# Kernel optimization log

Measured on AMD Instinct MI355X. Metric: run time of the kernel, lower is better.

Reference implementation:

```python
import jax, jax.numpy as jnp
import numpy as np

N, G, L, C = 32768, 128, 256, 128   # nodes, graphs, nodes-per-graph, channels
E, DS, DC, DR = 524288, 16, 4, 8    # edges, d_state, d_conv, dt_rank
EPS = 1e-5


def setup_inputs():
    key = jax.random.key(0)
    ks = jax.random.split(key, 16)
    s = 0.02
    p = lambda i, shape: jax.random.normal(ks[i], shape, jnp.float32) * s
    return {
        "x": jax.random.normal(ks[0], (N, C), jnp.float32),
        "edge_index": jax.random.randint(ks[1], (2, E), 0, N),
        "batch": jnp.repeat(jnp.arange(G), L),  # uniform graph sizes, sorted
        "gin_eps": jnp.float32(0.0),
        "gin_w1": p(2, (C, C)), "gin_b1": jnp.zeros((C,), jnp.float32),
        "gin_w2": p(3, (C, C)), "gin_b2": jnp.zeros((C,), jnp.float32),
        "in_proj_w": p(4, (2 * C, C)),
        "conv_w": p(5, (C, DC)), "conv_b": jnp.zeros((C,), jnp.float32),
        "x_proj_w": p(6, (DR + 2 * DS, C)),
        "dt_proj_w": p(7, (C, DR)),
        "dt_proj_b": jnp.full((C,), -4.0, jnp.float32),  # softplus -> small dt
        "A_log": jnp.log(jnp.broadcast_to(jnp.arange(1, DS + 1, dtype=jnp.float32), (C, DS))),
        "Dp": jnp.ones((C,), jnp.float32),
        "out_proj_w": p(8, (C, C)),
        "mlp_w1": p(9, (2 * C, C)), "mlp_b1": jnp.zeros((2 * C,), jnp.float32),
        "mlp_w2": p(10, (C, 2 * C)), "mlp_b2": jnp.zeros((C,), jnp.float32),
        "g1": jnp.ones((C,), jnp.float32), "be1": jnp.zeros((C,), jnp.float32),
        "g2": jnp.ones((C,), jnp.float32), "be2": jnp.zeros((C,), jnp.float32),
        "g3": jnp.ones((C,), jnp.float32), "be3": jnp.zeros((C,), jnp.float32),
    }


def batch_norm(h, g, b):
    # BatchNorm1d forward (batch statistics, biased var), eps=1e-5
    mu = h.mean(0)
    var = h.var(0)
    return (h - mu) * jax.lax.rsqrt(var + EPS) * g + b


def mamba(xd, in_proj_w, conv_w, conv_b, x_proj_w, dt_proj_w, dt_proj_b, A_log, Dp, out_proj_w):
    # xd: [G, L, C]; Mamba with expand=1 (d_inner == C)
    xz = jnp.einsum('glc,dc->gld', xd, in_proj_w)        # [G,L,2C]
    xs, z = jnp.split(xz, 2, axis=-1)
    # depthwise causal conv1d, kernel DC, left-pad DC-1
    xc = jax.lax.conv_general_dilated(
        xs.transpose(0, 2, 1), conv_w[:, None, :], (1,), [(DC - 1, 0)],
        dimension_numbers=('NCH', 'OIH', 'NCH'), feature_group_count=C)
    xs = jax.nn.silu(xc.transpose(0, 2, 1) + conv_b)     # [G,L,C]
    xdbl = jnp.einsum('gld,ed->gle', xs, x_proj_w)       # [G,L,DR+2*DS]
    dtr, Bm, Cm = jnp.split(xdbl, [DR, DR + DS], axis=-1)
    dt = jax.nn.softplus(jnp.einsum('glr,dr->gld', dtr, dt_proj_w) + dt_proj_b)  # [G,L,C]
    A = -jnp.exp(A_log)                                   # [C,DS]

    def step(hst, t):
        dt_t, B_t, C_t, x_t = t                           # [G,C],[G,DS],[G,DS],[G,C]
        dA = jnp.exp(dt_t[..., None] * A)                 # [G,C,DS]
        hst = dA * hst + dt_t[..., None] * B_t[:, None, :] * x_t[..., None]
        return hst, (hst * C_t[:, None, :]).sum(-1)       # y_t: [G,C]

    h0 = jnp.zeros((G, C, DS), xd.dtype)
    _, y = jax.lax.scan(step, h0, (dt.transpose(1, 0, 2), Bm.transpose(1, 0, 2),
                                   Cm.transpose(1, 0, 2), xs.transpose(1, 0, 2)))
    y = y.transpose(1, 0, 2) + Dp * xs                    # [G,L,C]
    y = y * jax.nn.silu(z)
    return jnp.einsum('gld,cd->glc', y, out_proj_w)


def _forward(edge_index, x, gin_eps, gin_w1, gin_b1, gin_w2, gin_b2,
             in_proj_w, conv_w, conv_b, x_proj_w, dt_proj_w, dt_proj_b,
             A_log, Dp, out_proj_w, mlp_w1, mlp_b1, mlp_w2, mlp_b2,
             g1, be1, g2, be2, g3, be3):
    # --- local MPNN branch: GIN conv + residual + norm1 (dropout=0, eval) ---
    agg = jax.ops.segment_sum(x[edge_index[0]], edge_index[1], num_segments=N)
    hg = (1.0 + gin_eps) * x + agg
    hg = jax.nn.relu(hg @ gin_w1.T + gin_b1) @ gin_w2.T + gin_b2
    h1 = batch_norm(hg + x, g1, be1)
    # --- Mamba branch over dense batch (uniform sizes -> reshape, mask all-true) ---
    xd = x.reshape(G, L, C)
    hm = mamba(xd, in_proj_w, conv_w, conv_b, x_proj_w, dt_proj_w, dt_proj_b,
               A_log, Dp, out_proj_w).reshape(N, C)
    h2 = batch_norm(hm + x, g2, be2)
    # --- combine + MLP + norm3 ---
    out = h1 + h2
    out = out + (jax.nn.relu(out @ mlp_w1.T + mlp_b1) @ mlp_w2.T + mlp_b2)
    out = batch_norm(out, g3, be3)
    return out, h2


def reference(x, edge_index, batch, gin_eps, gin_w1, gin_b1, gin_w2, gin_b2,
              in_proj_w, conv_w, conv_b, x_proj_w, dt_proj_w, dt_proj_b,
              A_log, Dp, out_proj_w, mlp_w1, mlp_b1, mlp_w2, mlp_b2,
              g1, be1, g2, be2, g3, be3):
    del batch  # uniform graph sizes encoded in (G, L)
    return _forward(edge_index, x, gin_eps, gin_w1, gin_b1, gin_w2, gin_b2,
                    in_proj_w, conv_w, conv_b, x_proj_w, dt_proj_w, dt_proj_b,
                    A_log, Dp, out_proj_w, mlp_w1, mlp_b1, mlp_w2, mlp_b2,
                    g1, be1, g2, be2, g3, be3)
```

## Files before the change

### kernel.cpp

```cpp
#include <hip/hip_runtime.h>
#include <hip/hip_bf16.h>

#define NN 32768
#define GG 128
#define LL 256
#define CC 128
#define EE 524288
#define NCHUNK 8
#define TCH 32

typedef __attribute__((ext_vector_type(8))) short short8v;
typedef __attribute__((ext_vector_type(4))) short short4v;
typedef __attribute__((ext_vector_type(4))) float floatx4;

__device__ inline short f2bf(float f) {
    __hip_bfloat16 h = __float2bfloat16(f);
    short s; __builtin_memcpy(&s, &h, 2); return s;
}
__device__ inline float b2f(unsigned short u) {
    unsigned v = ((unsigned)u) << 16; float f; __builtin_memcpy(&f, &v, 4); return f;
}
__device__ inline floatx4 mfma16(short8v a, short8v b, floatx4 c) {
    return __builtin_amdgcn_mfma_f32_16x16x32_bf16(a, b, c, 0, 0, 0);
}
__device__ inline float softplus_f(float v) {
    return (v > 20.f) ? v : __logf(1.f + __expf(v));
}

__global__ __launch_bounds__(256)
void prep_kernel(const float* __restrict__ x,
                 const float* __restrict__ gw1, const float* __restrict__ gw2,
                 const float* __restrict__ ipw, const float* __restrict__ xpw,
                 const float* __restrict__ opw, const float* __restrict__ mw1,
                 const float* __restrict__ mw2, const float* __restrict__ dtw,
                 unsigned short* __restrict__ wb, int* __restrict__ cnt,
                 float* __restrict__ stats, unsigned short* __restrict__ xb)
{
    int b = blockIdx.x, tid = threadIdx.x;
    if (b < 74) {
        const float* src; int dstoff, lb;
        if (b < 8)       { src = gw1;        dstoff = 0;      lb = b; }
        else if (b < 16) { src = gw2;        dstoff = 16384;  lb = b - 8; }
        else if (b < 32) { src = ipw;        dstoff = 32768;  lb = b - 16; }
        else if (b < 34) { src = xpw + 1024; dstoff = 81920;  lb = b - 32; }
        else if (b < 42) { src = opw;        dstoff = 86016;  lb = b - 34; }
        else if (b < 58) { src = mw1;        dstoff = 102400; lb = b - 42; }
        else             { src = mw2;        dstoff = 135168; lb = b - 58; }
        size_t i = (size_t)lb * 2048 + tid * 8;
        float4 a = *(const float4*)(src + i);
        float4 c = *(const float4*)(src + i + 4);
        short8v s = { f2bf(a.x), f2bf(a.y), f2bf(a.z), f2bf(a.w),
                      f2bf(c.x), f2bf(c.y), f2bf(c.z), f2bf(c.w) };
        *(short8v*)(wb + dstoff + i) = s;
    } else if (b < 138) {
        int i = (b - 74) * 256 + tid;
        int d = i >> 7, c = i & 127;
        float s = 0.f;
#pragma unroll
        for (int r = 0; r < 8; r++) s = fmaf(dtw[d * 8 + r], xpw[r * 128 + c], s);
        wb[65536 + i] = (unsigned short)f2bf(s);
    } else if (b < 170) {
        int idx = (b - 138) * 1024 + tid * 4;
        *(int4*)(cnt + idx) = make_int4(0, 0, 0, 0);
    } else if (b == 170) {
        stats[tid] = 0.f; stats[256 + tid] = 0.f; stats[512 + tid] = 0.f;
    } else {
        size_t i = (size_t)(b - 171) * 256 + tid;
        float4 a = *(const float4*)(x + i * 8);
        float4 c = *(const float4*)(x + i * 8 + 4);
        short8v s = { f2bf(a.x), f2bf(a.y), f2bf(a.z), f2bf(a.w),
                      f2bf(c.x), f2bf(c.y), f2bf(c.z), f2bf(c.w) };
        *(short8v*)(xb + i * 8) = s;
    }
}

__global__ __launch_bounds__(256)
void front_hist_kernel(const unsigned short* __restrict__ xb,
                 const unsigned short* __restrict__ ipwb,
                 const float* __restrict__ cw, const float* __restrict__ cb,
                 const unsigned short* __restrict__ wdtb, const float* __restrict__ dtbv,
                 const unsigned short* __restrict__ xpwb,
                 const float* __restrict__ Alog,
                 unsigned short* __restrict__ xsb, unsigned short* __restrict__ zb,
                 unsigned short* __restrict__ dtout, float* __restrict__ BCout,
                 float* __restrict__ Q, float* __restrict__ SDT,
                 const int* __restrict__ ei, int* __restrict__ cnt)
{
    __shared__ __align__(16) unsigned char smem[48 * 136 * 2 + 32 * 136 * 2 + TCH * 16 * 4];
    const int tid = threadIdx.x;
    if (blockIdx.x >= 1024) {
        int e = (blockIdx.x - 1024) * 256 + tid;
        atomicAdd(&cnt[ei[EE + e]], 1);
        return;
    }
    unsigned short* xsL = (unsigned short*)smem;
    unsigned short* xcL = xsL + 48 * 136;
    float* BsL = (float*)(xcL + 32 * 136);
    const int lane = tid & 63;
    const int wv = tid >> 6;
    const int rql = lane & 15;
    const int kseg = (lane >> 4) * 8;
    const int rsub = (lane >> 4) * 4;
    const int fb = blockIdx.x;
    const int R0 = fb * 32;
    const int RB = R0 - 16;
    const int g = fb >> 3;
    const int chunk = fb & 7;

    int coln[4];
#pragma unroll
    for (int n = 0; n < 4; n++) coln[n] = wv * 64 + n * 16 + rql;
    short8v wr[4][4];
#pragma unroll
    for (int n = 0; n < 4; n++) {
        const unsigned short* wp = ipwb + (size_t)coln[n] * 128 + kseg;
#pragma unroll
        for (int kk = 0; kk < 4; kk++) wr[n][kk] = *(const short8v*)(wp + kk * 32);
    }
    int arow[3];
#pragma unroll
    for (int m = 0; m < 3; m++) {
        int r = RB + m * 16 + rql;
        arow[m] = r < 0 ? 0 : r;
    }
    floatx4 acc[3][4];
#pragma unroll
    for (int m = 0; m < 3; m++)
#pragma unroll
        for (int n = 0; n < 4; n++)
#pragma unroll
            for (int r = 0; r < 4; r++) acc[m][n][r] = 0.f;
#pragma unroll
    for (int kb = 0; kb < 4; kb += 2) {
        short8v a2[3][2];
#pragma unroll
        for (int m = 0; m < 3; m++)
#pragma unroll
            for (int j = 0; j < 2; j++)
                a2[m][j] = *(const short8v*)(xb + (size_t)arow[m] * 128 + kseg + (kb + j) * 32);
        __builtin_amdgcn_sched_barrier(0);
#pragma unroll
        for (int j = 0; j < 2; j++)
#pragma unroll
            for (int m = 0; m < 3; m++)
#pragma unroll
                for (int n = 0; n < 4; n++)
                    acc[m][n] = mfma16(a2[m][j], wr[n][kb + j], acc[m][n]);
    }
    if (wv < 2) {
#pragma unroll
        for (int m = 0; m < 3; m++)
#pragma unroll
            for (int r = 0; r < 4; r++) {
                int row_l = m * 16 + rsub + r;
#pragma unroll
                for (int n = 0; n < 4; n++)
                    xsL[row_l * 136 + coln[n]] = (unsigned short)f2bf(acc[m][n][r]);
            }
    } else {
#pragma unroll
        for (int m = 1; m < 3; m++)
#pragma unroll
            for (int r = 0; r < 4; r++) {
                int row_g = RB + m * 16 + rsub + r;
#pragma unroll
                for (int n = 0; n < 4; n++)
                    zb[(size_t)row_g * 128 + (coln[n] - 128)] = (unsigned short)f2bf(acc[m][n][r]);
            }
    }
    __syncthreads();

    {
        int r = tid >> 3;
        int c0 = (tid & 7) * 16;
        int l = (R0 + r) & (LL - 1);
        const unsigned short* basep = &xsL[(16 + r) * 136 + c0];
        unsigned short o16[16];
#pragma unroll
        for (int half = 0; half < 2; half++) {
            short8v x0 = *(const short8v*)(basep + half * 8);
            short8v x1 = *(const short8v*)(basep - 136 + half * 8);
            short8v x2 = *(const short8v*)(basep - 272 + half * 8);
            short8v x3 = *(const short8v*)(basep - 408 + half * 8);
#pragma unroll
            for (int j = 0; j < 8; j++) {
                int c = c0 + half * 8 + j;
                float4 w = *(const float4*)(cw + c * 4);
                float v = cb[c];
                v = fmaf(b2f((unsigned short)x0[j]), w.w, v);
                if (l >= 1) v = fmaf(b2f((unsigned short)x1[j]), w.z, v);
                if (l >= 2) v = fmaf(b2f((unsigned short)x2[j]), w.y, v);
                if (l >= 3) v = fmaf(b2f((unsigned short)x3[j]), w.x, v);
                v = v / (1.f + __expf(-v));
                o16[half * 8 + j] = (unsigned short)f2bf(v);
            }
        }
#pragma unroll
        for (int half = 0; half < 2; half++) {
            short8v s;
#pragma unroll
            for (int j = 0; j < 8; j++) s[j] = (short)o16[half * 8 + j];
            *(short8v*)&xcL[r * 136 + c0 + half * 8] = s;
            *(short8v*)(xsb + (size_t)(R0 + r) * 128 + c0 + half * 8) = s;
        }
    }
    __syncthreads();

    unsigned short* dtL = xsL;
    int cold0 = wv * 32 + rql, cold1 = cold0 + 16;
    short8v wd0[4], wd1[4];
    {
        const unsigned short* wp0 = wdtb + (size_t)cold0 * 128 + kseg;
        const unsigned short* wp1 = wdtb + (size_t)cold1 * 128 + kseg;
#pragma unroll
        for (int kk = 0; kk < 4; kk++) {
            wd0[kk] = *(const short8v*)(wp0 + kk * 32);
            wd1[kk] = *(const short8v*)(wp1 + kk * 32);
        }
    }
    float bd0 = dtbv[cold0], bd1 = dtbv[cold1];
    int colb = wv * 16 + rql;
    short8v wbc[4];
    if (wv < 2) {
        const unsigned short* wp = xpwb + (size_t)colb * 128 + kseg;
#pragma unroll
        for (int kk = 0; kk < 4; kk++) wbc[kk] = *(const short8v*)(wp + kk * 32);
    }
    short8v a0[4], a1[4];
#pragma unroll
    for (int kk = 0; kk < 4; kk++) {
        a0[kk] = *(const short8v*)&xcL[rql * 136 + kseg + kk * 32];
        a1[kk] = *(const short8v*)&xcL[(16 + rql) * 136 + kseg + kk * 32];
    }
    floatx4 accd[2][2], accb[2];
#pragma unroll
    for (int m = 0; m < 2; m++) {
#pragma unroll
        for (int n = 0; n < 2; n++)
#pragma unroll
            for (int r = 0; r < 4; r++) accd[m][n][r] = 0.f;
#pragma unroll
        for (int r = 0; r < 4; r++) accb[m][r] = 0.f;
    }
#pragma unroll
    for (int kk = 0; kk < 4; kk++) {
        accd[0][0] = mfma16(a0[kk], wd0[kk], accd[0][0]);
        accd[0][1] = mfma16(a0[kk], wd1[kk], accd[0][1]);
        accd[1][0] = mfma16(a1[kk], wd0[kk], accd[1][0]);
        accd[1][1] = mfma16(a1[kk], wd1[kk], accd[1][1]);
        if (wv < 2) {
            accb[0] = mfma16(a0[kk], wbc[kk], accb[0]);
            accb[1] = mfma16(a1[kk], wbc[kk], accb[1]);
        }
    }
#pragma unroll
    for (int m = 0; m < 2; m++) {
#pragma unroll
        for (int r = 0; r < 4; r++) {
            int tl = m * 16 + rsub + r;
            int row_g = R0 + tl;
            float v0 = softplus_f(accd[m][0][r] + bd0);
            float v1 = softplus_f(accd[m][1][r] + bd1);
            unsigned short u0 = (unsigned short)f2bf(v0);
            unsigned short u1 = (unsigned short)f2bf(v1);
            dtout[(size_t)row_g * 128 + cold0] = u0;
            dtout[(size_t)row_g * 128 + cold1] = u1;
            dtL[tl * 136 + cold0] = u0;
            dtL[tl * 136 + cold1] = u1;
            if (wv < 2) {
                BCout[(size_t)row_g * 32 + colb] = accb[m][r];
                if (wv == 0) BsL[tl * 16 + colb] = accb[m][r];
            }
        }
    }
    __syncthreads();

    for (int u = tid; u < 512; u += 256) {
        int c = u >> 2, sp = u & 3;
        float ae0 = -__expf(Alog[c * 16 + sp * 4 + 0]);
        float ae1 = -__expf(Alog[c * 16 + sp * 4 + 1]);
        float ae2 = -__expf(Alog[c * 16 + sp * 4 + 2]);
        float ae3 = -__expf(Alog[c * 16 + sp * 4 + 3]);
        float q0 = 0, q1 = 0, q2 = 0, q3 = 0, sdt = 0;
        for (int t = TCH - 1; t >= 0; --t) {
            float dtv = b2f(dtL[t * 136 + c]);
            float xv  = b2f(xcL[t * 136 + c]);
            float uu = dtv * xv;
            const float* bs = &BsL[t * 16 + sp * 4];
            q0 = fmaf(__expf(ae0 * sdt) * uu, bs[0], q0);
            q1 = fmaf(__expf(ae1 * sdt) * uu, bs[1], q1);
            q2 = fmaf(__expf(ae2 * sdt) * uu, bs[2], q2);
            q3 = fmaf(__expf(ae3 * sdt) * uu, bs[3], q3);
            sdt += dtv;
        }
        float4* qp = (float4*)(Q + (((size_t)g * NCHUNK + chunk) * CC + c) * 16 + sp * 4);
        *qp = make_float4(q0, q1, q2, q3);
        if (sp == 0) SDT[((size_t)g * NCHUNK + chunk) * CC + c] = sdt;
    }
}

__global__ __launch_bounds__(1024)
void scanB_kernel(const int* __restrict__ cnt, int* __restrict__ base,
                  int* __restrict__ cursor,
                  const float* __restrict__ Q, const float* __restrict__ SDT,
                  const float* __restrict__ Alog, float* __restrict__ Hin)
{
    int tid = threadIdx.x;
    if (blockIdx.x == 0) {
        __shared__ int part[1024];
        int local[32];
        int s = 0;
#pragma unroll
        for (int j = 0; j < 32; j++) { local[j] = cnt[tid * 32 + j]; s += local[j]; }
        part[tid] = s;
        __syncthreads();
        for (int off = 1; off < 1024; off <<= 1) {
            int v = (tid >= off) ? part[tid - off] : 0;
            __syncthreads();
            part[tid] += v;
            __syncthreads();
        }
        int run = part[tid] - s;
#pragma unroll
        for (int j = 0; j < 32; j++) {
            base[tid * 32 + j] = run;
            cursor[tid * 32 + j] = run;
            run += local[j];
        }
        if (tid == 0) base[NN] = EE;
        return;
    }
    int idx = (blockIdx.x - 1) * 1024 + tid;
    int g = idx >> 11;
    int cs = idx & 2047;
    float ae = -__expf(Alog[cs]);
    float h = 0.f;
#pragma unroll
    for (int k = 0; k < NCHUNK; k++) {
        size_t o = ((size_t)g * NCHUNK + k);
        Hin[o * 2048 + cs] = h;
        float sdt = SDT[o * CC + (cs >> 4)];
        h = fmaf(__expf(ae * sdt), h, Q[o * 2048 + cs]);
    }
}

__global__ __launch_bounds__(256) void permute_kernel(const int* __restrict__ ei,
    int* __restrict__ cursor, int* __restrict__ perm)
{
    int e = blockIdx.x * 256 + threadIdx.x;
    int dst = ei[EE + e];
    int pos = atomicAdd(&cursor[dst], 1);
    perm[pos] = ei[e];
}

__global__ __launch_bounds__(512)
void scanout_gather_kernel(const float* __restrict__ BCp,
    const unsigned short* __restrict__ dtp, const unsigned short* __restrict__ xsp_,
    const unsigned short* __restrict__ zb, const float* __restrict__ Alog,
    const float* __restrict__ Dp, const float* __restrict__ Hin,
    const unsigned short* __restrict__ opwb, const unsigned short* __restrict__ xb,
    float* __restrict__ p2, float* ssum, float* ssq,
    const int* __restrict__ perm, const int* __restrict__ base,
    const float* __restrict__ epsp, unsigned short* __restrict__ hgin)
{
    __shared__ __align__(16) unsigned char smem[31232];
    const int tid = threadIdx.x;
    if (blockIdx.x >= 1024) {
        int node = (blockIdx.x - 1024) * 32 + (tid >> 4);
        int c8 = tid & 15;
        int b0 = base[node], b1 = base[node + 1];
        float s[8] = {0,0,0,0,0,0,0,0};
        float t[8] = {0,0,0,0,0,0,0,0};
        int i = b0;
        for (; i + 1 < b1; i += 2) {
            short8v v0 = *(const short8v*)(xb + (size_t)perm[i] * CC + c8 * 8);
            short8v v1 = *(const short8v*)(xb + (size_t)perm[i + 1] * CC + c8 * 8);
#pragma unroll
            for (int j = 0; j < 8; j++) {
                s[j] += b2f((unsigned short)v0[j]);
                t[j] += b2f((unsigned short)v1[j]);
            }
        }
        if (i < b1) {
            short8v v0 = *(const short8v*)(xb + (size_t)perm[i] * CC + c8 * 8);
#pragma unroll
            for (int j = 0; j < 8; j++) s[j] += b2f((unsigned short)v0[j]);
        }
        float e1 = 1.f + epsp[0];
        short8v xv = *(const short8v*)(xb + (size_t)node * CC + c8 * 8);
        short8v o;
#pragma unroll
        for (int j = 0; j < 8; j++)
            o[j] = f2bf(fmaf(e1, b2f((unsigned short)xv[j]), s[j] + t[j]));
        *(short8v*)(hgin + (size_t)node * CC + c8 * 8) = o;
        return;
    }
    float* BCs = (float*)smem;
    unsigned short* dts = (unsigned short*)(smem + 4096);
    unsigned short* xss = (unsigned short*)(smem + 12800);
    unsigned short* yL  = (unsigned short*)(smem + 21504);
    float* sred = (float*)(smem + 30208);
    const int b = blockIdx.x;
    const int g = b >> 3, chunk = b & 7;
    const int t0 = chunk * TCH;
    if (tid < 256) sred[tid] = 0.f;
    for (int i4 = tid; i4 < TCH * 8; i4 += 512) {
        int t = i4 >> 3, j4 = i4 & 7;
        *(float4*)&BCs[t * 32 + j4 * 4] =
            *(const float4*)(BCp + (size_t)(g * LL + t0 + t) * 32 + j4 * 4);
    }
    {
        int t = tid >> 4, c8 = tid & 15;
        size_t off = (size_t)(g * LL + t0 + t) * CC + c8 * 8;
        *(short8v*)&dts[t * 136 + c8 * 8] = *(const short8v*)(dtp + off);
        *(short8v*)&xss[t * 136 + c8 * 8] = *(const short8v*)(xsp_ + off);
    }
    const int c = tid >> 2, sp = tid & 3;
    float ae0 = -__expf(Alog[c * 16 + sp * 4 + 0]);
    float ae1 = -__expf(Alog[c * 16 + sp * 4 + 1]);
    float ae2 = -__expf(Alog[c * 16 + sp * 4 + 2]);
    float ae3 = -__expf(Alog[c * 16 + sp * 4 + 3]);
    float dpc = Dp[c];
    float4 hv = *(const float4*)(Hin + ((size_t)g * NCHUNK + chunk) * 2048 + c * 16 + sp * 4);
    float h0 = hv.x, h1 = hv.y, h2 = hv.z, h3 = hv.w;
    __syncthreads();
    const unsigned short* zg = zb + (size_t)(g * LL + t0) * CC + c;
    for (int t = 0; t < TCH; t++) {
        float dtv = b2f(dts[t * 136 + c]);
        float xv  = b2f(xss[t * 136 + c]);
        float u = dtv * xv;
        const float* bc = &BCs[t * 32 + sp * 4];
        h0 = fmaf(__expf(dtv * ae0), h0, u * bc[0]);
        h1 = fmaf(__expf(dtv * ae1), h1, u * bc[1]);
        h2 = fmaf(__expf(dtv * ae2), h2, u * bc[2]);
        h3 = fmaf(__expf(dtv * ae3), h3, u * bc[3]);
        float y = h0 * bc[16] + h1 * bc[17] + h2 * bc[18] + h3 * bc[19];
        y += __shfl_xor(y, 1);
        y += __shfl_xor(y, 2);
        if (sp == 0) {
            float zv = b2f(zg[t * CC]);
            float yo = fmaf(dpc, xv, y);
            yL[t * 136 + c] = (unsigned short)f2bf(yo * (zv / (1.f + __expf(-zv))));
        }
    }
    __syncthreads();

    const int lane = tid & 63;
    const int wv = tid >> 6;
    const int rql = lane & 15;
    const int kseg = (lane >> 4) * 8;
    const int rsub = (lane >> 4) * 4;
    const int colg = wv * 16 + rql;
    short8v w[4];
    {
        const unsigned short* wp = opwb + (size_t)colg * 128 + kseg;
#pragma unroll
        for (int kk = 0; kk < 4; kk++) w[kk] = *(const short8v*)(wp + kk * 32);
    }
    floatx4 acc[2];
#pragma unroll
    for (int m = 0; m < 2; m++)
#pragma unroll
        for (int r = 0; r < 4; r++) acc[m][r] = 0.f;
#pragma unroll
    for (int kk = 0; kk < 4; kk++) {
        short8v alo = *(const short8v*)&yL[rql * 136 + kseg + kk * 32];
        short8v ahi = *(const short8v*)&yL[(16 + rql) * 136 + kseg + kk * 32];
        acc[0] = mfma16(alo, w[kk], acc[0]);
        acc[1] = mfma16(ahi, w[kk], acc[1]);
    }
    float sumr = 0.f, sqr = 0.f;
#pragma unroll
    for (int m = 0; m < 2; m++) {
#pragma unroll
        for (int r = 0; r < 4; r++) {
            int row_g = g * LL + t0 + m * 16 + rsub + r;
            float v = acc[m][r] + b2f(xb[(size_t)row_g * CC + colg]);
            p2[(size_t)row_g * CC + colg] = v;
            sumr += v; sqr += v * v;
        }
    }
    sumr += __shfl_xor(sumr, 16); sumr += __shfl_xor(sumr, 32);
    sqr  += __shfl_xor(sqr, 16);  sqr  += __shfl_xor(sqr, 32);
    if ((lane >> 4) == 0) {
        atomicAdd(&sred[colg], sumr);
        atomicAdd(&sred[128 + colg], sqr);
    }
    __syncthreads();
    if (tid < 128) {
        atomicAdd(&ssum[tid], sred[tid]);
        atomicAdd(&ssq[tid], sred[128 + tid]);
    }
}

template<int KMID>
__global__ __launch_bounds__(256)
void fused2(const unsigned short* __restrict__ A,
            const unsigned short* __restrict__ W1b, const float* __restrict__ b1,
            const unsigned short* __restrict__ W2b, const float* __restrict__ b2,
            const unsigned short* __restrict__ residb,
            float* __restrict__ outp,
            float* ssum, float* ssq)
{
    constexpr int NF1 = KMID / 64;
    constexpr int NK1 = 4;
    constexpr int NK2 = KMID / 32;
    constexpr int LDSW = KMID + 8;
    __shared__ unsigned short lds[2][32 * LDSW];
    __shared__ float sred[256];
    const int tid = threadIdx.x;
    const int lane = tid & 63;
    const int wc = tid >> 6;
    const int rql = lane & 15;
    const int kseg = (lane >> 4) * 8;
    const int rsub = (lane >> 4) * 4;

    sred[tid] = 0.f;

    short8v w1r[NF1][NK1];
    int colg1[NF1];
    float b1c[NF1];
#pragma unroll
    for (int f = 0; f < NF1; f++) {
        colg1[f] = wc * (16 * NF1) + f * 16 + rql;
        const unsigned short* wp = W1b + (size_t)colg1[f] * 128 + kseg;
#pragma unroll
        for (int kk = 0; kk < NK1; kk++) w1r[f][kk] = *(const short8v*)(wp + kk * 32);
        b1c[f] = b1[colg1[f]];
    }
    int colg2[2];
    colg2[0] = wc * 32 + rql;
    colg2[1] = colg2[0] + 16;
    float b2c[2] = { b2[colg2[0]], b2[colg2[1]] };
    float ssumr[2] = {0.f, 0.f}, ssqr[2] = {0.f, 0.f};

    short8v abuf[2][NK1][2];
    {
        const unsigned short* ap = A + (size_t)(blockIdx.x * 32 + rql) * 128 + kseg;
#pragma unroll
        for (int kk = 0; kk < NK1; kk++) {
            abuf[0][kk][0] = *(const short8v*)(ap + kk * 32);
            abuf[0][kk][1] = *(const short8v*)(ap + 16 * 128 + kk * 32);
        }
    }
    __syncthreads();

#pragma unroll
    for (int t = 0; t < 2; t++) {
        const int R0 = (blockIdx.x + t * 512) * 32;
        floatx4 acc1[2][NF1];
#pragma unroll
        for (int m = 0; m < 2; m++)
#pragma unroll
            for (int f = 0; f < NF1; f++)
#pragma unroll
                for (int r = 0; r < 4; r++) acc1[m][f][r] = 0.f;
#pragma unroll
        for (int kk = 0; kk < NK1; kk++)
#pragma unroll
            for (int m = 0; m < 2; m++)
#pragma unroll
                for (int f = 0; f < NF1; f++)
                    acc1[m][f] = mfma16(abuf[t][kk][m], w1r[f][kk], acc1[m][f]);
        unsigned short* L = &lds[t][0];
#pragma unroll
        for (int m = 0; m < 2; m++)
#pragma unroll
            for (int f = 0; f < NF1; f++)
#pragma unroll
                for (int r = 0; r < 4; r++) {
                    float v = fmaxf(acc1[m][f][r] + b1c[f], 0.f);
                    L[(m * 16 + rsub + r) * LDSW + colg1[f]] = (unsigned short)f2bf(v);
                }
        __syncthreads();
        if (t == 0) {
            const unsigned short* ap = A + (size_t)((blockIdx.x + 512) * 32 + rql) * 128 + kseg;
#pragma unroll
            for (int kk = 0; kk < NK1; kk++) {
                abuf[1][kk][0] = *(const short8v*)(ap + kk * 32);
                abuf[1][kk][1] = *(const short8v*)(ap + 16 * 128 + kk * 32);
            }
        }
        short8v w2a[NK2], w2b[NK2];
        {
            const unsigned short* wq0 = W2b + (size_t)colg2[0] * KMID + kseg;
            const unsigned short* wq1 = W2b + (size_t)colg2[1] * KMID + kseg;
#pragma unroll
            for (int kk = 0; kk < NK2; kk++) {
                w2a[kk] = *(const short8v*)(wq0 + kk * 32);
                w2b[kk] = *(const short8v*)(wq1 + kk * 32);
            }
        }
        floatx4 acc2[2][2];
#pragma unroll
        for (int m = 0; m < 2; m++)
#pragma unroll
            for (int n = 0; n < 2; n++)
#pragma unroll
                for (int r = 0; r < 4; r++) acc2[m][n][r] = 0.f;
#pragma unroll
        for (int kk = 0; kk < NK2; kk++) {
            short8v a2lo = *(const short8v*)&L[rql * LDSW + kseg + kk * 32];
            short8v a2hi = *(const short8v*)&L[(rql + 16) * LDSW + kseg + kk * 32];
            acc2[0][0] = mfma16(a2lo, w2a[kk], acc2[0][0]);
            acc2[0][1] = mfma16(a2lo, w2b[kk], acc2[0][1]);
            acc2[1][0] = mfma16(a2hi, w2a[kk], acc2[1][0]);
            acc2[1][1] = mfma16(a2hi, w2b[kk], acc2[1][1]);
        }
#pragma unroll
        for (int m = 0; m < 2; m++) {
#pragma unroll
            for (int r = 0; r < 4; r++) {
                int row_g = R0 + m * 16 + rsub + r;
#pragma unroll
                for (int n = 0; n < 2; n++) {
                    float v = acc2[m][n][r] + b2c[n];
                    v += b2f(residb[(size_t)row_g * CC + colg2[n]]);
                    outp[(size_t)row_g * CC + colg2[n]] = v;
                    ssumr[n] += v; ssqr[n] += v * v;
                }
            }
        }
    }
    __syncthreads();
#pragma unroll
    for (int n = 0; n < 2; n++) {
        atomicAdd(&sred[colg2[n]], ssumr[n]);
        atomicAdd(&sred[128 + colg2[n]], ssqr[n]);
    }
    __syncthreads();
    if (tid < 128) {
        atomicAdd(&ssum[tid], sred[tid]);
        atomicAdd(&ssq[tid], sred[128 + tid]);
    }
}

__global__ __launch_bounds__(256) void norm12_kernel(const float* __restrict__ p1,
    const float* __restrict__ p2, const float* __restrict__ stats,
    const float* g1, const float* be1, const float* g2, const float* be2,
    float* __restrict__ h2out, unsigned short* __restrict__ out12b)
{
    __shared__ float sc[512];
    int tid = threadIdx.x;
    if (tid < 128) {
        int c = tid;
        const float inv = 1.0f / NN;
        float m1 = stats[c] * inv;
        float v1 = fmaxf(stats[128 + c] * inv - m1 * m1, 0.f);
        float i1 = rsqrtf(v1 + 1e-5f);
        sc[c] = g1[c] * i1; sc[128 + c] = be1[c] - m1 * g1[c] * i1;
        float m2 = stats[256 + c] * inv;
        float v2 = fmaxf(stats[384 + c] * inv - m2 * m2, 0.f);
        float i2 = rsqrtf(v2 + 1e-5f);
        sc[256 + c] = g2[c] * i2; sc[384 + c] = be2[c] - m2 * g2[c] * i2;
    }
    __syncthreads();
    size_t idx = (size_t)blockIdx.x * 256 + tid;
    int c4 = (int)(idx & 31);
    float4 s1 = *(float4*)&sc[c4 * 4];
    float4 t1 = *(float4*)&sc[128 + c4 * 4];
    float4 s2 = *(float4*)&sc[256 + c4 * 4];
    float4 t2 = *(float4*)&sc[384 + c4 * 4];
    float4 a = *(const float4*)(p1 + idx * 4);
    float4 b = *(const float4*)(p2 + idx * 4);
    float4 h, o;
    h.x = fmaf(b.x, s2.x, t2.x); o.x = fmaf(a.x, s1.x, t1.x) + h.x;
    h.y = fmaf(b.y, s2.y, t2.y); o.y = fmaf(a.y, s1.y, t1.y) + h.y;
    h.z = fmaf(b.z, s2.z, t2.z); o.z = fmaf(a.z, s1.z, t1.z) + h.z;
    h.w = fmaf(b.w, s2.w, t2.w); o.w = fmaf(a.w, s1.w, t1.w) + h.w;
    *(float4*)(h2out + idx * 4) = h;
    short4v ob = { f2bf(o.x), f2bf(o.y), f2bf(o.z), f2bf(o.w) };
    *(short4v*)(out12b + idx * 4) = ob;
}

__global__ __launch_bounds__(256) void norm3_kernel(const float* __restrict__ p3,
    const float* __restrict__ stats, const float* g3, const float* be3,
    float* __restrict__ outp)
{
    __shared__ float sc[256];
    int tid = threadIdx.x;
    if (tid < 128) {
        int c = tid;
        const float inv = 1.0f / NN;
        float m = stats[512 + c] * inv;
        float v = fmaxf(stats[640 + c] * inv - m * m, 0.f);
        float iv = rsqrtf(v + 1e-5f);
        sc[c] = g3[c] * iv; sc[128 + c] = be3[c] - m * g3[c] * iv;
    }
    __syncthreads();
    size_t idx = (size_t)blockIdx.x * 256 + tid;
    int c4 = (int)(idx & 31);
    float4 s = *(float4*)&sc[c4 * 4];
    float4 t = *(float4*)&sc[128 + c4 * 4];
    float4 a = *(const float4*)(p3 + idx * 4);
    float4 o;
    o.x = fmaf(a.x, s.x, t.x); o.y = fmaf(a.y, s.y, t.y);
    o.z = fmaf(a.z, s.z, t.z); o.w = fmaf(a.w, s.w, t.w);
    *(float4*)(outp + idx * 4) = o;
}

extern "C" void kernel_launch(void* const* d_in, const int* in_sizes, int n_in,
                              void* d_out, int out_size, void* d_ws, size_t ws_size,
                              hipStream_t stream)
{
    (void)in_sizes; (void)n_in; (void)out_size; (void)ws_size;
    const float* x    = (const float*)d_in[0];
    const int*   ei   = (const int*)d_in[1];
    const float* eps  = (const float*)d_in[3];
    const float* gw1  = (const float*)d_in[4];
    const float* gb1  = (const float*)d_in[5];
    const float* gw2  = (const float*)d_in[6];
    const float* gb2  = (const float*)d_in[7];
    const float* ipw  = (const float*)d_in[8];
    const float* cw   = (const float*)d_in[9];
    const float* cb   = (const float*)d_in[10];
    const float* xpw  = (const float*)d_in[11];
    const float* dtw  = (const float*)d_in[12];
    const float* dtb  = (const float*)d_in[13];
    const float* Alog = (const float*)d_in[14];
    const float* Dp   = (const float*)d_in[15];
    const float* opw  = (const float*)d_in[16];
    const float* mw1  = (const float*)d_in[17];
    const float* mb1  = (const float*)d_in[18];
    const float* mw2  = (const float*)d_in[19];
    const float* mb2  = (const float*)d_in[20];
    const float* g1   = (const float*)d_in[21];
    const float* be1  = (const float*)d_in[22];
    const float* g2   = (const float*)d_in[23];
    const float* be2  = (const float*)d_in[24];
    const float* g3   = (const float*)d_in[25];
    const float* be3  = (const float*)d_in[26];

    float* outp = (float*)d_out;
    float* h2o  = outp + (size_t)NN * CC;
    float* p1 = outp;
    float* p2 = h2o;

    const size_t M1 = 1u << 20;
    float* ws = (float*)d_ws;
    float*  scr4   = ws;
    float*  BC     = ws + 4 * M1;
    unsigned short* zb      = (unsigned short*)(ws + 7 * M1);
    unsigned short* dtb_buf = (unsigned short*)(ws + 9 * M1);
    unsigned short* xb      = (unsigned short*)(ws + 11 * M1);
    unsigned short* hgin    = (unsigned short*)(ws + 13 * M1);
    unsigned short* xsb     = (unsigned short*)(ws + 15 * M1);
    unsigned short* out12b  = (unsigned short*)(ws + 17 * M1);
    float*  stats  = ws + 19 * M1;
    int*    cnt    = (int*)(stats + 768);
    int*    baseA  = cnt + NN;
    int*    cursor = baseA + NN + 1;
    int*    perm   = cursor + NN;
    float*  SDT    = (float*)(perm + EE);
    unsigned short* wbase = (unsigned short*)(SDT + 131072);
    unsigned short* gw1b = wbase;
    unsigned short* gw2b = wbase + 16384;
    unsigned short* ipwb = wbase + 32768;
    unsigned short* wdtb = wbase + 65536;
    unsigned short* xpwb = wbase + 81920;
    unsigned short* opwb = wbase + 86016;
    unsigned short* mw1b = wbase + 102400;
    unsigned short* mw2b = wbase + 135168;

    float* Qbuf = scr4;
    float* Hin  = scr4 + 2 * M1;
    float* p3   = scr4;

    prep_kernel<<<dim3(171 + 2048), 256, 0, stream>>>(
        x, gw1, gw2, ipw, xpw, opw, mw1, mw2, dtw, wbase, cnt, stats, xb);

    front_hist_kernel<<<dim3(3072), 256, 0, stream>>>(
        xb, ipwb, cw, cb, wdtb, dtb, xpwb, Alog, xsb, zb, dtb_buf, BC, Qbuf, SDT,
        ei, cnt);

    scanB_kernel<<<dim3(257), 1024, 0, stream>>>(cnt, baseA, cursor, Qbuf, SDT, Alog, Hin);

    permute_kernel<<<dim3(EE / 256), 256, 0, stream>>>(ei, cursor, perm);

    scanout_gather_kernel<<<dim3(2048), 512, 0, stream>>>(
        BC, dtb_buf, xsb, zb, Alog, Dp, Hin, opwb, xb, p2, stats + 256, stats + 384,
        perm, baseA, eps, hgin);

    fused2<128><<<dim3(512), 256, 0, stream>>>(
        hgin, gw1b, gb1, gw2b, gb2, xb, p1, stats + 0, stats + 128);

    norm12_kernel<<<dim3(NN * CC / 4 / 256), 256, 0, stream>>>(
        p1, p2, stats, g1, be1, g2, be2, h2o, out12b);

    fused2<256><<<dim3(512), 256, 0, stream>>>(
        out12b, mw1b, mb1, mw2b, mb2, out12b, p3, stats + 512, stats + 640);

    norm3_kernel<<<dim3(NN * CC / 4 / 256), 256, 0, stream>>>(p3, stats, g3, be3, outp);
}
```

Before: 243.6 us.

## Widen front kernel to 512 threads and use running decay product in chunk scan

Doubles the front_hist block size to 8 waves, splitting the in_proj, conv, and dt_proj MFMA work across twice as many waves, each holding half the weight registers. The histogram blocks now cover 512 edges each, so fewer blocks are launched. The per-chunk state reduction replaces exp(A*cumulative_dt) per step with a running product multiplied by exp(A*dt). The intent is more latency hiding and lower register pressure per wave. The trade-offs are an extra sync cost across more waves and slightly different floating-point rounding in the decay products.

```diff
diff --git a/kernel.cpp b/kernel.cpp
--- a/kernel.cpp
+++ b/kernel.cpp
@@ -74,7 +74,7 @@
     }
 }
 
-__global__ __launch_bounds__(256)
+__global__ __launch_bounds__(512)
 void front_hist_kernel(const unsigned short* __restrict__ xb,
                  const unsigned short* __restrict__ ipwb,
                  const float* __restrict__ cw, const float* __restrict__ cb,
@@ -89,7 +89,7 @@
     __shared__ __align__(16) unsigned char smem[48 * 136 * 2 + 32 * 136 * 2 + TCH * 16 * 4];
     const int tid = threadIdx.x;
     if (blockIdx.x >= 1024) {
-        int e = (blockIdx.x - 1024) * 256 + tid;
+        int e = (blockIdx.x - 1024) * 512 + tid;
         atomicAdd(&cnt[ei[EE + e]], 1);
         return;
     }
@@ -107,12 +107,12 @@
     const int g = fb >> 3;
     const int chunk = fb & 7;
 
-    int coln[4];
-#pragma unroll
-    for (int n = 0; n < 4; n++) coln[n] = wv * 64 + n * 16 + rql;
-    short8v wr[4][4];
-#pragma unroll
-    for (int n = 0; n < 4; n++) {
+    int coln[2];
+    coln[0] = wv * 32 + rql;
+    coln[1] = coln[0] + 16;
+    short8v wr[2][4];
+#pragma unroll
+    for (int n = 0; n < 2; n++) {
         const unsigned short* wp = ipwb + (size_t)coln[n] * 128 + kseg;
 #pragma unroll
         for (int kk = 0; kk < 4; kk++) wr[n][kk] = *(const short8v*)(wp + kk * 32);
@@ -123,11 +123,11 @@
         int r = RB + m * 16 + rql;
         arow[m] = r < 0 ? 0 : r;
     }
-    floatx4 acc[3][4];
+    floatx4 acc[3][2];
 #pragma unroll
     for (int m = 0; m < 3; m++)
 #pragma unroll
-        for (int n = 0; n < 4; n++)
+        for (int n = 0; n < 2; n++)
 #pragma unroll
             for (int r = 0; r < 4; r++) acc[m][n][r] = 0.f;
 #pragma unroll
@@ -144,17 +144,17 @@
 #pragma unroll
             for (int m = 0; m < 3; m++)
 #pragma unroll
-                for (int n = 0; n < 4; n++)
+                for (int n = 0; n < 2; n++)
                     acc[m][n] = mfma16(a2[m][j], wr[n][kb + j], acc[m][n]);
     }
-    if (wv < 2) {
+    if (wv < 4) {
 #pragma unroll
         for (int m = 0; m < 3; m++)
 #pragma unroll
             for (int r = 0; r < 4; r++) {
                 int row_l = m * 16 + rsub + r;
 #pragma unroll
-                for (int n = 0; n < 4; n++)
+                for (int n = 0; n < 2; n++)
                     xsL[row_l * 136 + coln[n]] = (unsigned short)f2bf(acc[m][n][r]);
             }
     } else {
@@ -164,61 +164,48 @@
             for (int r = 0; r < 4; r++) {
                 int row_g = RB + m * 16 + rsub + r;
 #pragma unroll
-                for (int n = 0; n < 4; n++)
+                for (int n = 0; n < 2; n++)
                     zb[(size_t)row_g * 128 + (coln[n] - 128)] = (unsigned short)f2bf(acc[m][n][r]);
             }
     }
     __syncthreads();
 
     {
-        int r = tid >> 3;
-        int c0 = (tid & 7) * 16;
+        int r = tid >> 4;
+        int c0 = (tid & 15) * 8;
         int l = (R0 + r) & (LL - 1);
         const unsigned short* basep = &xsL[(16 + r) * 136 + c0];
-        unsigned short o16[16];
-#pragma unroll
-        for (int half = 0; half < 2; half++) {
-            short8v x0 = *(const short8v*)(basep + half * 8);
-            short8v x1 = *(const short8v*)(basep - 136 + half * 8);
-            short8v x2 = *(const short8v*)(basep - 272 + half * 8);
-            short8v x3 = *(const short8v*)(basep - 408 + half * 8);
-#pragma unroll
-            for (int j = 0; j < 8; j++) {
-                int c = c0 + half * 8 + j;
-                float4 w = *(const float4*)(cw + c * 4);
-                float v = cb[c];
-                v = fmaf(b2f((unsigned short)x0[j]), w.w, v);
-                if (l >= 1) v = fmaf(b2f((unsigned short)x1[j]), w.z, v);
-                if (l >= 2) v = fmaf(b2f((unsigned short)x2[j]), w.y, v);
-                if (l >= 3) v = fmaf(b2f((unsigned short)x3[j]), w.x, v);
-                v = v / (1.f + __expf(-v));
-                o16[half * 8 + j] = (unsigned short)f2bf(v);
-            }
-        }
-#pragma unroll
-        for (int half = 0; half < 2; half++) {
-            short8v s;
-#pragma unroll
-            for (int j = 0; j < 8; j++) s[j] = (short)o16[half * 8 + j];
-            *(short8v*)&xcL[r * 136 + c0 + half * 8] = s;
-            *(short8v*)(xsb + (size_t)(R0 + r) * 128 + c0 + half * 8) = s;
-        }
+        short8v x0 = *(const short8v*)basep;
+        short8v x1 = *(const short8v*)(basep - 136);
+        short8v x2 = *(const short8v*)(basep - 272);
+        short8v x3 = *(const short8v*)(basep - 408);
+        short8v s;
+#pragma unroll
+        for (int j = 0; j < 8; j++) {
+            int c = c0 + j;
+            float4 w = *(const float4*)(cw + c * 4);
+            float v = cb[c];
+            v = fmaf(b2f((unsigned short)x0[j]), w.w, v);
+            if (l >= 1) v = fmaf(b2f((unsigned short)x1[j]), w.z, v);
+            if (l >= 2) v = fmaf(b2f((unsigned short)x2[j]), w.y, v);
+            if (l >= 3) v = fmaf(b2f((unsigned short)x3[j]), w.x, v);
+            v = v / (1.f + __expf(-v));
+            s[j] = f2bf(v);
+        }
+        *(short8v*)&xcL[r * 136 + c0] = s;
+        *(short8v*)(xsb + (size_t)(R0 + r) * 128 + c0) = s;
     }
     __syncthreads();
 
     unsigned short* dtL = xsL;
-    int cold0 = wv * 32 + rql, cold1 = cold0 + 16;
-    short8v wd0[4], wd1[4];
+    int cold = wv * 16 + rql;
+    short8v wd[4];
     {
-        const unsigned short* wp0 = wdtb + (size_t)cold0 * 128 + kseg;
-        const unsigned short* wp1 = wdtb + (size_t)cold1 * 128 + kseg;
-#pragma unroll
-        for (int kk = 0; kk < 4; kk++) {
-            wd0[kk] = *(const short8v*)(wp0 + kk * 32);
-            wd1[kk] = *(const short8v*)(wp1 + kk * 32);
-        }
-    }
-    float bd0 = dtbv[cold0], bd1 = dtbv[cold1];
+        const unsigned short* wp = wdtb + (size_t)cold * 128 + kseg;
+#pragma unroll
+        for (int kk = 0; kk < 4; kk++) wd[kk] = *(const short8v*)(wp + kk * 32);
+    }
+    float bd = dtbv[cold];
     int colb = wv * 16 + rql;
     short8v wbc[4];
     if (wv < 2) {
@@ -232,22 +219,15 @@
         a0[kk] = *(const short8v*)&xcL[rql * 136 + kseg + kk * 32];
         a1[kk] = *(const short8v*)&xcL[(16 + rql) * 136 + kseg + kk * 32];
     }
-    floatx4 accd[2][2], accb[2];
-#pragma unroll
-    for (int m = 0; m < 2; m++) {
-#pragma unroll
-        for (int n = 0; n < 2; n++)
-#pragma unroll
-            for (int r = 0; r < 4; r++) accd[m][n][r] = 0.f;
-#pragma unroll
-        for (int r = 0; r < 4; r++) accb[m][r] = 0.f;
-    }
+    floatx4 accd[2], accb[2];
+#pragma unroll
+    for (int m = 0; m < 2; m++)
+#pragma unroll
+        for (int r = 0; r < 4; r++) { accd[m][r] = 0.f; accb[m][r] = 0.f; }
 #pragma unroll
     for (int kk = 0; kk < 4; kk++) {
-        accd[0][0] = mfma16(a0[kk], wd0[kk], accd[0][0]);
-        accd[0][1] = mfma16(a0[kk], wd1[kk], accd[0][1]);
-        accd[1][0] = mfma16(a1[kk], wd0[kk], accd[1][0]);
-        accd[1][1] = mfma16(a1[kk], wd1[kk], accd[1][1]);
+        accd[0] = mfma16(a0[kk], wd[kk], accd[0]);
+        accd[1] = mfma16(a1[kk], wd[kk], accd[1]);
         if (wv < 2) {
             accb[0] = mfma16(a0[kk], wbc[kk], accb[0]);
             accb[1] = mfma16(a1[kk], wbc[kk], accb[1]);
@@ -259,14 +239,10 @@
         for (int r = 0; r < 4; r++) {
             int tl = m * 16 + rsub + r;
             int row_g = R0 + tl;
-            float v0 = softplus_f(accd[m][0][r] + bd0);
-            float v1 = softplus_f(accd[m][1][r] + bd1);
+            float v0 = softplus_f(accd[m][r] + bd);
             unsigned short u0 = (unsigned short)f2bf(v0);
-            unsigned short u1 = (unsigned short)f2bf(v1);
-            dtout[(size_t)row_g * 128 + cold0] = u0;
-            dtout[(size_t)row_g * 128 + cold1] = u1;
-            dtL[tl * 136 + cold0] = u0;
-            dtL[tl * 136 + cold1] = u1;
+            dtout[(size_t)row_g * 128 + cold] = u0;
+            dtL[tl * 136 + cold] = u0;
             if (wv < 2) {
                 BCout[(size_t)row_g * 32 + colb] = accb[m][r];
                 if (wv == 0) BsL[tl * 16 + colb] = accb[m][r];
@@ -275,27 +251,28 @@
     }
     __syncthreads();
 
-    for (int u = tid; u < 512; u += 256) {
-        int c = u >> 2, sp = u & 3;
-        float ae0 = -__expf(Alog[c * 16 + sp * 4 + 0]);
-        float ae1 = -__expf(Alog[c * 16 + sp * 4 + 1]);
-        float ae2 = -__expf(Alog[c * 16 + sp * 4 + 2]);
-        float ae3 = -__expf(Alog[c * 16 + sp * 4 + 3]);
-        float q0 = 0, q1 = 0, q2 = 0, q3 = 0, sdt = 0;
+    {
+        int c0_ = tid >> 2, sp = tid & 3;
+        float ae[4];
+#pragma unroll
+        for (int j = 0; j < 4; j++) ae[j] = -__expf(Alog[c0_ * 16 + sp * 4 + j]);
+        float q[4] = {0.f, 0.f, 0.f, 0.f};
+        float p[4] = {1.f, 1.f, 1.f, 1.f};
+        float sdt = 0.f;
         for (int t = TCH - 1; t >= 0; --t) {
-            float dtv = b2f(dtL[t * 136 + c]);
-            float xv  = b2f(xcL[t * 136 + c]);
-            float uu = dtv * xv;
+            float dtv = b2f(dtL[t * 136 + c0_]);
+            float uu = dtv * b2f(xcL[t * 136 + c0_]);
             const float* bs = &BsL[t * 16 + sp * 4];
-            q0 = fmaf(__expf(ae0 * sdt) * uu, bs[0], q0);
-            q1 = fmaf(__expf(ae1 * sdt) * uu, bs[1], q1);
-            q2 = fmaf(__expf(ae2 * sdt) * uu, bs[2], q2);
-            q3 = fmaf(__expf(ae3 * sdt) * uu, bs[3], q3);
+#pragma unroll
+            for (int j = 0; j < 4; j++) {
+                q[j] = fmaf(p[j] * uu, bs[j], q[j]);
+                p[j] *= __expf(ae[j] * dtv);
+            }
             sdt += dtv;
         }
-        float4* qp = (float4*)(Q + (((size_t)g * NCHUNK + chunk) * CC + c) * 16 + sp * 4);
-        *qp = make_float4(q0, q1, q2, q3);
-        if (sp == 0) SDT[((size_t)g * NCHUNK + chunk) * CC + c] = sdt;
+        size_t obase = ((size_t)g * NCHUNK + chunk);
+        *(float4*)(Q + (obase * CC + c0_) * 16 + sp * 4) = make_float4(q[0], q[1], q[2], q[3]);
+        if (sp == 0) SDT[obase * CC + c0_] = sdt;
     }
 }
 
@@ -769,7 +746,7 @@
     prep_kernel<<<dim3(171 + 2048), 256, 0, stream>>>(
         x, gw1, gw2, ipw, xpw, opw, mw1, mw2, dtw, wbase, cnt, stats, xb);
 
-    front_hist_kernel<<<dim3(3072), 256, 0, stream>>>(
+    front_hist_kernel<<<dim3(2048), 512, 0, stream>>>(
         xb, ipwb, cw, cb, wdtb, dtb, xpwb, Alog, xsb, zb, dtb_buf, BC, Qbuf, SDT,
         ei, cnt);
 
```

After: 247.8 us. About the same (+1.7%).
